# Optimization experiments

Measured on AMD Instinct MI355X. Metric: run time of the kernel, lower is better.

## Reference

```python
import jax, jax.numpy as jnp
import numpy as np

N, M, P = 64, 64, 64
T = 262144

def setup_inputs() -> dict:
    key = jax.random.key(0)
    ks = jax.random.split(key, 6)
    return {
        "u": jax.random.normal(ks[0], (T, M), dtype=jnp.float32),
        "x0": jax.random.normal(ks[1], (N,), dtype=jnp.float32),
        "A": jax.random.normal(ks[2], (N, N), dtype=jnp.float32) * 0.1,
        "B": jax.random.normal(ks[3], (N, M), dtype=jnp.float32) * 0.1,
        "C": jax.random.normal(ks[4], (P, N), dtype=jnp.float32) * 0.1,
        "D": jax.random.normal(ks[5], (P, M), dtype=jnp.float32) * 0.1,
    }

def reference(u, x0, A, B, C, D):
    # Precompute input drives in one big GEMM each: Bu[k] = B @ u[k], Du[k] = D @ u[k]
    Bu = u @ B.T            # (T, n)
    Du = u @ D.T            # (T, p)

    def step(x, bu):
        # y_k uses pre-update state x_k; next state x_{k+1} = A x_k + B u_k
        x_next = A @ x + bu
        return x_next, x     # carry new state, emit x_k

    _, xs = jax.lax.scan(step, x0, Bu)   # xs: (T, n) = [x_0 ... x_{T-1}]
    ys = xs @ C.T + Du                   # (T, p)
    return ys
```

## Files before the change

kernel.cpp:

```cpp
#include <hip/hip_runtime.h>


#define T_LEN  262144
#define NTAP   33
#define ZLEN   48
#define ROWS   512
#define HALO   32

typedef __attribute__((ext_vector_type(8))) short  short8;
typedef __attribute__((ext_vector_type(4))) float  floatx4;

static __device__ __forceinline__ unsigned short f2bf(float f) {
    unsigned int x = __float_as_uint(f);
    x += 0x7fffu + ((x >> 16) & 1u);
    return (unsigned short)(x >> 16);
}
static __device__ __forceinline__ float bf2f(unsigned short u) {
    return __uint_as_float(((unsigned int)u) << 16);
}

__global__ __launch_bounds__(256, 1) void k_prep(
    const float* __restrict__ A, const float* __restrict__ B,
    const float* __restrict__ C, const float* __restrict__ D,
    const float* __restrict__ x0, unsigned short* __restrict__ gG,
    float* __restrict__ gZ)
{
    __shared__ unsigned short At[64][72];
    __shared__ unsigned short Bt[64][72];
    __shared__ unsigned short M0[64][72];
    __shared__ unsigned short M1[64][72];
    const int tid = threadIdx.x;
    const int wv = tid >> 6, lane = tid & 63, l15 = lane & 15, q = lane >> 4;

#pragma unroll
    for (int e = 0; e < 16; ++e) {
        int f = e * 256 + tid;
        int r = f >> 6, cc = f & 63;
        At[cc][r] = f2bf(A[f]);
        Bt[cc][r] = f2bf(B[f]);
        M0[r][cc] = f2bf(C[f]);
        gG[f]     = f2bf(D[f]);
    }
    __syncthreads();

    float x0v[4];
#pragma unroll
    for (int nt = 0; nt < 4; ++nt) x0v[nt] = x0[l15 + 16 * nt];

    short8 bA[2][4], bB[2][4];
#pragma unroll
    for (int kb = 0; kb < 2; ++kb)
#pragma unroll
        for (int nt = 0; nt < 4; ++nt) {
            bA[kb][nt] = *(const short8*)&At[l15 + 16*nt][kb*32 + q*8];
            bB[kb][nt] = *(const short8*)&Bt[l15 + 16*nt][kb*32 + q*8];
        }

#pragma unroll
    for (int r = 0; r < 4; ++r) {
        float v = 0.f;
#pragma unroll
        for (int nt = 0; nt < 4; ++nt)
            v += bf2f(M0[16*wv + q*4 + r][l15 + 16*nt]) * x0v[nt];
        v += __shfl_xor(v, 1, 16); v += __shfl_xor(v, 2, 16);
        v += __shfl_xor(v, 4, 16); v += __shfl_xor(v, 8, 16);
        if (l15 == 0) gZ[16*wv + q*4 + r] = v;
    }

    unsigned short (*Ms)[72] = M0;
    unsigned short (*Md)[72] = M1;
    for (int i = 1; i < ZLEN; ++i) {
        short8 a0 = *(const short8*)&Ms[16*wv + l15][q*8];
        short8 a1 = *(const short8*)&Ms[16*wv + l15][32 + q*8];

        if (i < NTAP) {
            floatx4 g[4];
#pragma unroll
            for (int nt = 0; nt < 4; ++nt) {
                g[nt] = (floatx4){0.f, 0.f, 0.f, 0.f};
                g[nt] = __builtin_amdgcn_mfma_f32_16x16x32_bf16(a0, bB[0][nt], g[nt], 0, 0, 0);
                g[nt] = __builtin_amdgcn_mfma_f32_16x16x32_bf16(a1, bB[1][nt], g[nt], 0, 0, 0);
            }
#pragma unroll
            for (int nt = 0; nt < 4; ++nt)
#pragma unroll
                for (int r = 0; r < 4; ++r)
                    gG[(size_t)i*4096 + (16*wv + q*4 + r)*64 + l15 + 16*nt] = f2bf(g[nt][r]);
        }

        floatx4 m[4];
#pragma unroll
        for (int nt = 0; nt < 4; ++nt) {
            m[nt] = (floatx4){0.f, 0.f, 0.f, 0.f};
            m[nt] = __builtin_amdgcn_mfma_f32_16x16x32_bf16(a0, bA[0][nt], m[nt], 0, 0, 0);
            m[nt] = __builtin_amdgcn_mfma_f32_16x16x32_bf16(a1, bA[1][nt], m[nt], 0, 0, 0);
        }
#pragma unroll
        for (int nt = 0; nt < 4; ++nt)
#pragma unroll
            for (int r = 0; r < 4; ++r)
                Md[16*wv + q*4 + r][l15 + 16*nt] = f2bf(m[nt][r]);

#pragma unroll
        for (int r = 0; r < 4; ++r) {
            float v = 0.f;
#pragma unroll
            for (int nt = 0; nt < 4; ++nt) v = fmaf(m[nt][r], x0v[nt], v);
            v += __shfl_xor(v, 1, 16); v += __shfl_xor(v, 2, 16);
            v += __shfl_xor(v, 4, 16); v += __shfl_xor(v, 8, 16);
            if (l15 == 0) gZ[i*64 + 16*wv + q*4 + r] = v;
        }

        unsigned short (*tmp)[72] = Ms; Ms = Md; Md = tmp;
    }
}

__device__ __forceinline__ void loadG(short8 (&b)[8],
                                      const unsigned short* __restrict__ gG,
                                      int i, int l15, int q)
{
#pragma unroll
    for (int kb = 0; kb < 2; ++kb)
#pragma unroll
        for (int nt = 0; nt < 4; ++nt)
            b[kb*4 + nt] = *(const short8*)(gG + (size_t)i*4096
                              + (l15 + 16*nt)*64 + kb*32 + q*8);
}

__device__ __forceinline__ void tapStep(floatx4 (&acc)[8][4],
                                        const unsigned short (*uS)[72],
                                        const short8 (&b)[8],
                                        int i, int wv, int l15, int q)
{
    const int rbase = wv*128 + l15 + HALO - i;
#pragma unroll
    for (int kb = 0; kb < 2; ++kb)
#pragma unroll
        for (int mt = 0; mt < 8; ++mt) {
            short8 a = *(const short8*)&uS[rbase + mt*16][kb*32 + q*8];
#pragma unroll
            for (int nt = 0; nt < 4; ++nt)
                acc[mt][nt] = __builtin_amdgcn_mfma_f32_16x16x32_bf16(
                    a, b[kb*4 + nt], acc[mt][nt], 0, 0, 0);
        }
}

__global__ __launch_bounds__(256, 2) void k_conv(
    const float* __restrict__ u, const unsigned short* __restrict__ gG,
    const float* __restrict__ gZ, float* __restrict__ out)
{
    __shared__ __align__(16) unsigned short uS[ROWS + HALO][72];
    const int tid = threadIdx.x;
    const int wv = tid >> 6, lane = tid & 63, l15 = lane & 15, q = lane >> 4;
    const int t0 = blockIdx.x * ROWS;

    {
        const float4* u4 = (const float4*)u;
        const int base4 = (t0 - HALO) * 16;
#pragma unroll
        for (int e = 0; e < 34; ++e) {
            int f = e * 256 + tid;
            float4 v = make_float4(0.f, 0.f, 0.f, 0.f);
            if (base4 + f >= 0) v = u4[base4 + f];
            int r = f >> 4, cx = (f & 15) * 4;
            uS[r][cx+0] = f2bf(v.x); uS[r][cx+1] = f2bf(v.y);
            uS[r][cx+2] = f2bf(v.z); uS[r][cx+3] = f2bf(v.w);
        }
    }
    __syncthreads();

    floatx4 acc[8][4];
#pragma unroll
    for (int mt = 0; mt < 8; ++mt)
#pragma unroll
        for (int nt = 0; nt < 4; ++nt) acc[mt][nt] = (floatx4){0.f, 0.f, 0.f, 0.f};

    short8 b0[8], b1[8];
    loadG(b0, gG, 0, l15, q);
    for (int ii = 0; ii < 16; ++ii) {
        loadG(b1, gG, 2*ii + 1, l15, q);
        tapStep(acc, uS, b0, 2*ii, wv, l15, q);
        loadG(b0, gG, 2*ii + 2, l15, q);
        tapStep(acc, uS, b1, 2*ii + 1, wv, l15, q);
    }
    tapStep(acc, uS, b0, 32, wv, l15, q);

    const bool zblk = (blockIdx.x == 0 && wv == 0);
#pragma unroll
    for (int mt = 0; mt < 8; ++mt)
#pragma unroll
        for (int nt = 0; nt < 4; ++nt) {
            const int p = l15 + 16*nt;
#pragma unroll
            for (int r = 0; r < 4; ++r) {
                int tl = wv*128 + mt*16 + q*4 + r;
                float v = acc[mt][nt][r];
                if (zblk && mt < 3) v += gZ[(mt*16 + q*4 + r)*64 + p];
                out[(size_t)(t0 + tl)*64 + p] = v;
            }
        }
}

extern "C" void kernel_launch(void* const* d_in, const int* in_sizes, int n_in,
                              void* d_out, int out_size, void* d_ws, size_t ws_size,
                              hipStream_t stream) {
    const float* u  = (const float*)d_in[0];
    const float* x0 = (const float*)d_in[1];
    const float* A  = (const float*)d_in[2];
    const float* B  = (const float*)d_in[3];
    const float* C  = (const float*)d_in[4];
    const float* D  = (const float*)d_in[5];
    float* out = (float*)d_out;

    unsigned short* gG = (unsigned short*)d_ws;
    float* gZ = (float*)((char*)d_ws + 272384);

    hipLaunchKernelGGL(k_prep, dim3(1), dim3(256), 0, stream,
                       A, B, C, D, x0, gG, gZ);
    hipLaunchKernelGGL(k_conv, dim3(T_LEN / ROWS), dim3(256), 0, stream,
                       u, gG, gZ, out);
}
```

Measured before the change: 239.6 us.

## Halve conv tile rows and move free-response reduction off the serial prep loop

The convolution kernel now handles 256 rows per block, each wave covering 64 rows instead of 128. This doubles the grid and halves the accumulator registers, so occupancy can rise to 3 blocks per CU at the price of a larger relative halo reload. The prep kernel stores each C*A^i power to workspace and computes the x0 response afterwards in a parallel pass, taking the shuffle reductions out of the serial power loop. That adds 48 small global writes and reads.

Result: slower. 317.9 us (+32.7%).

```diff
diff --git a/kernel.cpp b/kernel.cpp
--- a/kernel.cpp
+++ b/kernel.cpp
@@ -4,7 +4,8 @@
 #define T_LEN  262144
 #define NTAP   33
 #define ZLEN   48
-#define ROWS   512
+#define ROWS   256
+#define WROWS  64
 #define HALO   32
 
 typedef __attribute__((ext_vector_type(8))) short  short8;
@@ -23,12 +24,13 @@
     const float* __restrict__ A, const float* __restrict__ B,
     const float* __restrict__ C, const float* __restrict__ D,
     const float* __restrict__ x0, unsigned short* __restrict__ gG,
-    float* __restrict__ gZ)
+    float* __restrict__ gZ, unsigned short* __restrict__ gM)
 {
     __shared__ unsigned short At[64][72];
     __shared__ unsigned short Bt[64][72];
     __shared__ unsigned short M0[64][72];
     __shared__ unsigned short M1[64][72];
+    __shared__ float x0s[64];
     const int tid = threadIdx.x;
     const int wv = tid >> 6, lane = tid & 63, l15 = lane & 15, q = lane >> 4;
 
@@ -38,14 +40,13 @@
         int r = f >> 6, cc = f & 63;
         At[cc][r] = f2bf(A[f]);
         Bt[cc][r] = f2bf(B[f]);
-        M0[r][cc] = f2bf(C[f]);
+        unsigned short cb = f2bf(C[f]);
+        M0[r][cc] = cb;
+        gM[f]     = cb;
         gG[f]     = f2bf(D[f]);
     }
+    if (tid < 64) x0s[tid] = x0[tid];
     __syncthreads();
-
-    float x0v[4];
-#pragma unroll
-    for (int nt = 0; nt < 4; ++nt) x0v[nt] = x0[l15 + 16 * nt];
 
     short8 bA[2][4], bB[2][4];
 #pragma unroll
@@ -55,17 +56,6 @@
             bA[kb][nt] = *(const short8*)&At[l15 + 16*nt][kb*32 + q*8];
             bB[kb][nt] = *(const short8*)&Bt[l15 + 16*nt][kb*32 + q*8];
         }
-
-#pragma unroll
-    for (int r = 0; r < 4; ++r) {
-        float v = 0.f;
-#pragma unroll
-        for (int nt = 0; nt < 4; ++nt)
-            v += bf2f(M0[16*wv + q*4 + r][l15 + 16*nt]) * x0v[nt];
-        v += __shfl_xor(v, 1, 16); v += __shfl_xor(v, 2, 16);
-        v += __shfl_xor(v, 4, 16); v += __shfl_xor(v, 8, 16);
-        if (l15 == 0) gZ[16*wv + q*4 + r] = v;
-    }
 
     unsigned short (*Ms)[72] = M0;
     unsigned short (*Md)[72] = M1;
@@ -73,6 +63,23 @@
         short8 a0 = *(const short8*)&Ms[16*wv + l15][q*8];
         short8 a1 = *(const short8*)&Ms[16*wv + l15][32 + q*8];
 
+        floatx4 m[4];
+#pragma unroll
+        for (int nt = 0; nt < 4; ++nt) {
+            m[nt] = (floatx4){0.f, 0.f, 0.f, 0.f};
+            m[nt] = __builtin_amdgcn_mfma_f32_16x16x32_bf16(a0, bA[0][nt], m[nt], 0, 0, 0);
+            m[nt] = __builtin_amdgcn_mfma_f32_16x16x32_bf16(a1, bA[1][nt], m[nt], 0, 0, 0);
+        }
+#pragma unroll
+        for (int nt = 0; nt < 4; ++nt)
+#pragma unroll
+            for (int r = 0; r < 4; ++r) {
+                unsigned short mb = f2bf(m[nt][r]);
+                int row = 16*wv + q*4 + r, col = l15 + 16*nt;
+                Md[row][col] = mb;
+                gM[(size_t)i*4096 + row*64 + col] = mb;
+            }
+
         if (i < NTAP) {
             floatx4 g[4];
 #pragma unroll
@@ -88,30 +95,16 @@
                     gG[(size_t)i*4096 + (16*wv + q*4 + r)*64 + l15 + 16*nt] = f2bf(g[nt][r]);
         }
 
-        floatx4 m[4];
-#pragma unroll
-        for (int nt = 0; nt < 4; ++nt) {
-            m[nt] = (floatx4){0.f, 0.f, 0.f, 0.f};
-            m[nt] = __builtin_amdgcn_mfma_f32_16x16x32_bf16(a0, bA[0][nt], m[nt], 0, 0, 0);
-            m[nt] = __builtin_amdgcn_mfma_f32_16x16x32_bf16(a1, bA[1][nt], m[nt], 0, 0, 0);
-        }
-#pragma unroll
-        for (int nt = 0; nt < 4; ++nt)
-#pragma unroll
-            for (int r = 0; r < 4; ++r)
-                Md[16*wv + q*4 + r][l15 + 16*nt] = f2bf(m[nt][r]);
-
-#pragma unroll
-        for (int r = 0; r < 4; ++r) {
-            float v = 0.f;
-#pragma unroll
-            for (int nt = 0; nt < 4; ++nt) v = fmaf(m[nt][r], x0v[nt], v);
-            v += __shfl_xor(v, 1, 16); v += __shfl_xor(v, 2, 16);
-            v += __shfl_xor(v, 4, 16); v += __shfl_xor(v, 8, 16);
-            if (l15 == 0) gZ[i*64 + 16*wv + q*4 + r] = v;
-        }
-
         unsigned short (*tmp)[72] = Ms; Ms = Md; Md = tmp;
+    }
+    __syncthreads();
+
+    for (int k = tid; k < ZLEN * 64; k += 256) {
+        const unsigned short* Mp = gM + (size_t)(k >> 6) * 4096 + (k & 63) * 64;
+        float v = 0.f;
+#pragma unroll
+        for (int mm = 0; mm < 64; ++mm) v = fmaf(bf2f(Mp[mm]), x0s[mm], v);
+        gZ[k] = v;
     }
 }
 
@@ -127,16 +120,16 @@
                               + (l15 + 16*nt)*64 + kb*32 + q*8);
 }
 
-__device__ __forceinline__ void tapStep(floatx4 (&acc)[8][4],
+__device__ __forceinline__ void tapStep(floatx4 (&acc)[4][4],
                                         const unsigned short (*uS)[72],
                                         const short8 (&b)[8],
                                         int i, int wv, int l15, int q)
 {
-    const int rbase = wv*128 + l15 + HALO - i;
+    const int rbase = wv*WROWS + l15 + HALO - i;
 #pragma unroll
     for (int kb = 0; kb < 2; ++kb)
 #pragma unroll
-        for (int mt = 0; mt < 8; ++mt) {
+        for (int mt = 0; mt < 4; ++mt) {
             short8 a = *(const short8*)&uS[rbase + mt*16][kb*32 + q*8];
 #pragma unroll
             for (int nt = 0; nt < 4; ++nt)
@@ -145,7 +138,7 @@
         }
 }
 
-__global__ __launch_bounds__(256, 2) void k_conv(
+__global__ __launch_bounds__(256, 3) void k_conv(
     const float* __restrict__ u, const unsigned short* __restrict__ gG,
     const float* __restrict__ gZ, float* __restrict__ out)
 {
@@ -158,7 +151,7 @@
         const float4* u4 = (const float4*)u;
         const int base4 = (t0 - HALO) * 16;
 #pragma unroll
-        for (int e = 0; e < 34; ++e) {
+        for (int e = 0; e < 18; ++e) {
             int f = e * 256 + tid;
             float4 v = make_float4(0.f, 0.f, 0.f, 0.f);
             if (base4 + f >= 0) v = u4[base4 + f];
@@ -169,9 +162,9 @@
     }
     __syncthreads();
 
-    floatx4 acc[8][4];
-#pragma unroll
-    for (int mt = 0; mt < 8; ++mt)
+    floatx4 acc[4][4];
+#pragma unroll
+    for (int mt = 0; mt < 4; ++mt)
 #pragma unroll
         for (int nt = 0; nt < 4; ++nt) acc[mt][nt] = (floatx4){0.f, 0.f, 0.f, 0.f};
 
@@ -187,13 +180,13 @@
 
     const bool zblk = (blockIdx.x == 0 && wv == 0);
 #pragma unroll
-    for (int mt = 0; mt < 8; ++mt)
+    for (int mt = 0; mt < 4; ++mt)
 #pragma unroll
         for (int nt = 0; nt < 4; ++nt) {
             const int p = l15 + 16*nt;
 #pragma unroll
             for (int r = 0; r < 4; ++r) {
-                int tl = wv*128 + mt*16 + q*4 + r;
+                int tl = wv*WROWS + mt*16 + q*4 + r;
                 float v = acc[mt][nt][r];
                 if (zblk && mt < 3) v += gZ[(mt*16 + q*4 + r)*64 + p];
                 out[(size_t)(t0 + tl)*64 + p] = v;
@@ -213,10 +206,11 @@
     float* out = (float*)d_out;
 
     unsigned short* gG = (unsigned short*)d_ws;
-    float* gZ = (float*)((char*)d_ws + 272384);
+    float*          gZ = (float*)((char*)d_ws + 272384);
+    unsigned short* gM = (unsigned short*)((char*)d_ws + 286720);
 
     hipLaunchKernelGGL(k_prep, dim3(1), dim3(256), 0, stream,
-                       A, B, C, D, x0, gG, gZ);
+                       A, B, C, D, x0, gG, gZ, gM);
     hipLaunchKernelGGL(k_conv, dim3(T_LEN / ROWS), dim3(256), 0, stream,
                        u, gG, gZ, out);
 }
```
